# Performance work log

Hardware: AMD Instinct MI355X
Metric: run time of the kernel (lower is better)

The kernel has to match this reference:

```python
import jax, jax.numpy as jnp
import numpy as np

N_ITEMS = 100000
N_INTENTS = 512
H = 128
ALPHA = 0.5
TOPK = 3  # torch code: sim.topk(3, 1)


def _leaky_relu(x):
    return jnp.where(x > 0, x, 0.2 * x)  # nn.LeakyReLU(0.2)


def setup_inputs() -> dict:
    key = jax.random.key(0)
    k0, k1, k2, k3, k4, k5 = jax.random.split(key, 6)
    s = 1.0 / np.sqrt(H)
    return {
        "item_emb": jax.random.normal(k0, (N_ITEMS, H), jnp.float32),
        "intent_emb": jax.random.normal(k1, (N_INTENTS, H), jnp.float32),
        "Wq": (jax.random.normal(k2, (H, H), jnp.float32) * s),  # lq.weight
        "Wk": (jax.random.normal(k3, (H, H), jnp.float32) * s),  # lk.weight
        "wa": (jax.random.normal(k4, (H,), jnp.float32) * s),    # la.weight (1,H)
        "wb": (jax.random.normal(k5, (H,), jnp.float32) * s),    # lb.weight (1,H)
        "n_items": N_ITEMS,
        "n_intents": N_INTENTS,
    }


def reference(item_emb, intent_emb, Wq, Wk, wa, wb, n_items, n_intents):
    h = item_emb.shape[1]
    # dense similarity + row softmax + top-3 sparsification (indices only matter downstream)
    sim = (item_emb @ Wq.T) @ (intent_emb @ Wk.T).T / jnp.sqrt(jnp.float32(h))
    sim = jax.nn.softmax(sim, axis=1)                      # [n_items, n_intents]
    _, topi = jax.lax.top_k(sim, TOPK)                     # [n_items, 3]
    edge_item = jnp.repeat(jnp.arange(n_items), TOPK)      # [E]
    edge_intent = topi.reshape(-1)                         # [E]

    # --- GNNCell ---
    # att1: edges oriented intent<-item, softmax per intent row (segment softmax)
    s1 = _leaky_relu((intent_emb[edge_intent] * item_emb[edge_item]) @ wa)  # [E]
    m1 = jax.ops.segment_max(s1, edge_intent, num_segments=n_intents)
    e1 = jnp.exp(s1 - m1[edge_intent])
    d1 = jax.ops.segment_sum(e1, edge_intent, num_segments=n_intents)
    w1 = e1 / d1[edge_intent]
    intent_new = jax.ops.segment_sum(w1[:, None] * item_emb[edge_item],
                                     edge_intent, num_segments=n_intents)  # [n_intents, H]

    # att2: edges oriented item<-intent; each item has exactly 3 edges -> softmax over axis 1
    s2 = _leaky_relu((item_emb[edge_item] * intent_new[edge_intent]) @ wb)
    w2 = jax.nn.softmax(s2.reshape(n_items, TOPK), axis=1)  # [n_items, 3]
    item_nei = jnp.einsum("nk,nkh->nh", w2, intent_new[topi])

    return ALPHA * item_emb + (1.0 - ALPHA) * item_nei
```

## Files before the change

### kernel.cpp

```cpp
#include <hip/hip_runtime.h>
#include <math.h>

#define N_ITEMS 100000
#define N_INT   512
#define H       128
#define KCH     16
#define NCH     (H/KCH)
#define IPB     16
#define IPW     4
#define TILE    512
#define MAXTILES 2048

typedef unsigned int u32;

__device__ __forceinline__ float wave_sum(float v) {
#pragma unroll
  for (int d = 1; d < 64; d <<= 1) v += __shfl_xor(v, d, 64);
  return v;
}

__global__ void k_projK(const float* __restrict__ intent, const float* __restrict__ Wk,
                        float* __restrict__ K) {
  __shared__ float row[H];
  int j = blockIdx.x, h = threadIdx.x;
  row[h] = intent[j * H + h];
  __syncthreads();
  float acc = 0.f;
#pragma unroll 8
  for (int k = 0; k < H; ++k) acc += row[k] * Wk[h * H + k];
  K[j * H + h] = acc;
}

__global__ void k_projM(const float* __restrict__ Wq, const float* __restrict__ K,
                        float* __restrict__ M) {
  __shared__ float row[H];
  int j = blockIdx.x, k = threadIdx.x;
  row[k] = K[j * H + k];
  __syncthreads();
  float acc = 0.f;
#pragma unroll 8
  for (int a = 0; a < H; ++a) acc += Wq[a * H + k] * row[a];
  M[k * N_INT + j] = acc * 0.08838834764831845f;
}

__global__ __launch_bounds__(256) void k_simtop(
    const float* __restrict__ item, const float* __restrict__ M,
    const float* __restrict__ intent, const float* __restrict__ wa,
    int* __restrict__ topi, float* __restrict__ s1buf, int* __restrict__ counts) {
  __shared__ float sm[KCH * N_INT];
  __shared__ float sit[IPB * KCH];
  const int tid = threadIdx.x;
  const int lane = tid & 63;
  const int wv = __builtin_amdgcn_readfirstlane(tid >> 6);
  const int ibase = blockIdx.x * IPB;
  const int iw = wv * IPW * KCH;

  float acc[IPW][8];
#pragma unroll
  for (int i = 0; i < IPW; ++i)
#pragma unroll
    for (int jj = 0; jj < 8; ++jj) acc[i][jj] = 0.f;

  for (int kc = 0; kc < NCH; ++kc) {
    __syncthreads();
#pragma unroll
    for (int t = 0; t < 8; ++t) {
      int off = wv * 2048 + t * 256;
      __builtin_amdgcn_global_load_lds(
          (const __attribute__((address_space(1))) u32*)(M + kc * (KCH * N_INT) + off + lane * 4),
          (__attribute__((address_space(3))) u32*)(sm + off), 16, 0, 0);
    }
    if (wv == 0) {
      __builtin_amdgcn_global_load_lds(
          (const __attribute__((address_space(1))) u32*)(item + (size_t)(ibase + (lane >> 2)) * H + kc * KCH + (lane & 3) * 4),
          (__attribute__((address_space(3))) u32*)(sit + lane * 4), 16, 0, 0);
    }
    __syncthreads();
#pragma unroll
    for (int q = 0; q < 4; ++q) {
#pragma unroll
      for (int kk = 0; kk < 4; ++kk) {
        const int krow = q * 4 + kk;
        const float* rp = sm + krow * N_INT + lane * 4;
        float4 m0 = *reinterpret_cast<const float4*>(rp);
        float4 m1 = *reinterpret_cast<const float4*>(rp + 256);
#pragma unroll
        for (int i = 0; i < IPW; ++i) {
          float a = sit[iw + i * KCH + krow];
          acc[i][0] += a * m0.x; acc[i][1] += a * m0.y;
          acc[i][2] += a * m0.z; acc[i][3] += a * m0.w;
          acc[i][4] += a * m1.x; acc[i][5] += a * m1.y;
          acc[i][6] += a * m1.z; acc[i][7] += a * m1.w;
        }
      }
    }
  }

  const float wal = wa[lane], wah = wa[64 + lane];
#pragma unroll
  for (int i = 0; i < IPW; ++i) {
    float tv0 = -INFINITY, tv1 = -INFINITY, tv2 = -INFINITY;
    int ti0 = 0x7fffffff, ti1 = 0x7fffffff, ti2 = 0x7fffffff;
    auto push = [&](float v, int j) {
      bool b2 = (v > tv2) || (v == tv2 && j < ti2);
      if (b2) {
        bool b1 = (v > tv1) || (v == tv1 && j < ti1);
        if (b1) {
          bool b0 = (v > tv0) || (v == tv0 && j < ti0);
          if (b0) { tv2 = tv1; ti2 = ti1; tv1 = tv0; ti1 = ti0; tv0 = v; ti0 = j; }
          else    { tv2 = tv1; ti2 = ti1; tv1 = v; ti1 = j; }
        } else    { tv2 = v; ti2 = j; }
      }
    };
#pragma unroll
    for (int jj = 0; jj < 8; ++jj) {
      int j = (jj < 4) ? (4 * lane + jj) : (256 + 4 * lane + (jj - 4));
      push(acc[i][jj], j);
    }
#pragma unroll
    for (int d = 1; d < 64; d <<= 1) {
      float ov0 = __shfl_xor(tv0, d, 64), ov1 = __shfl_xor(tv1, d, 64), ov2 = __shfl_xor(tv2, d, 64);
      int   oi0 = __shfl_xor(ti0, d, 64), oi1 = __shfl_xor(ti1, d, 64), oi2 = __shfl_xor(ti2, d, 64);
      push(ov0, oi0); push(ov1, oi1); push(ov2, oi2);
    }
    const int gi = ibase + wv * IPW + i;
    const float itl = item[(size_t)gi * H + lane], ith = item[(size_t)gi * H + 64 + lane];
    const float pl = itl * wal, ph = ith * wah;
    int jsel[3] = {ti0, ti1, ti2};
#pragma unroll
    for (int e = 0; e < 3; ++e) {
      int j = jsel[e];
      float s = pl * intent[j * H + lane] + ph * intent[j * H + 64 + lane];
      s = wave_sum(s);
      s = (s > 0.f) ? s : 0.2f * s;
      if (lane == 0) {
        topi[gi * 3 + e] = j;
        s1buf[gi * 3 + e] = s;
        atomicAdd(&counts[j], 1);
      }
    }
  }
}

__global__ void k_scan(const int* __restrict__ counts, int* __restrict__ offs,
                       int* __restrict__ cursor, int* __restrict__ descs,
                       int* __restrict__ ntl) {
  __shared__ int s[N_INT];
  __shared__ int base;
  int t = threadIdx.x;
  if (t == 0) base = 0;
  int c = counts[t];
  s[t] = c;
  __syncthreads();
  for (int off = 1; off < N_INT; off <<= 1) {
    int v = (t >= off) ? s[t - off] : 0;
    __syncthreads();
    s[t] += v;
    __syncthreads();
  }
  int excl = s[t] - c;
  offs[t] = excl;
  cursor[t] = excl;
  if (t == N_INT - 1) offs[N_INT] = s[t];
  int nt = (c + TILE - 1) / TILE;
  int my = atomicAdd(&base, nt);
  for (int k = 0; k < nt; ++k) {
    descs[2 * (my + k)] = t;
    descs[2 * (my + k) + 1] = excl + k * TILE;
  }
  __syncthreads();
  if (t == 0) ntl[0] = base;
}

__global__ void k_scatter(const int* __restrict__ topi, const float* __restrict__ s1buf,
                          int* __restrict__ cursor, int* __restrict__ eitem,
                          float* __restrict__ es1) {
  int gi = blockIdx.x * 256 + threadIdx.x;
  if (gi >= N_ITEMS) return;
#pragma unroll
  for (int e = 0; e < 3; ++e) {
    int j = topi[gi * 3 + e];
    int pos = atomicAdd(&cursor[j], 1);
    eitem[pos] = gi;
    es1[pos] = s1buf[gi * 3 + e];
  }
}

__global__ __launch_bounds__(256) void k_agg(
    const float* __restrict__ item, const int* __restrict__ offs,
    const int* __restrict__ descs, const int* __restrict__ ntl,
    const int* __restrict__ eitem, const float* __restrict__ es1,
    float* __restrict__ num, float* __restrict__ denom) {
  int bt = blockIdx.x;
  if (bt >= ntl[0]) return;
  int j = descs[2 * bt];
  int beg = descs[2 * bt + 1];
  int end = min(offs[j + 1], beg + TILE);
  __shared__ float red[256];
  __shared__ float rd[2];
  int t = threadIdx.x;
  int h = t & 127, sub = t >> 7;
  float acc = 0.f, dp = 0.f;
  const float* ip = item + h;
#pragma unroll 4
  for (int e = beg + sub; e < end; e += 2) {
    float e1 = expf(es1[e]);
    acc += e1 * ip[(size_t)eitem[e] * H];
    dp += e1;
  }
  red[t] = acc;
  if (h == 0) rd[sub] = dp;
  __syncthreads();
  if (t < 128) atomicAdd(&num[j * H + t], red[t] + red[t + 128]);
  if (t == 0) atomicAdd(&denom[j], rd[0] + rd[1]);
}

__global__ __launch_bounds__(256) void k_final(
    const float* __restrict__ item, const int* __restrict__ topi,
    const float* __restrict__ num, const float* __restrict__ denom,
    const float* __restrict__ wb, float* __restrict__ out) {
  int tid = threadIdx.x;
  int lane = tid & 63;
  int wv = __builtin_amdgcn_readfirstlane(tid >> 6);
  int gi = blockIdx.x * 4 + wv;
  const float il = item[(size_t)gi * H + lane], ih = item[(size_t)gi * H + 64 + lane];
  const float wbl = wb[lane], wbh = wb[64 + lane];
  int j0 = topi[gi * 3 + 0], j1 = topi[gi * 3 + 1], j2 = topi[gi * 3 + 2];
  float d0 = denom[j0], d1 = denom[j1], d2 = denom[j2];
  float r0 = d0 > 0.f ? 1.f / d0 : 0.f;
  float r1 = d1 > 0.f ? 1.f / d1 : 0.f;
  float r2 = d2 > 0.f ? 1.f / d2 : 0.f;
  float n0l = num[j0 * H + lane] * r0, n0h = num[j0 * H + 64 + lane] * r0;
  float n1l = num[j1 * H + lane] * r1, n1h = num[j1 * H + 64 + lane] * r1;
  float n2l = num[j2 * H + lane] * r2, n2h = num[j2 * H + 64 + lane] * r2;
  float s0 = wave_sum(il * n0l * wbl + ih * n0h * wbh);
  float s1 = wave_sum(il * n1l * wbl + ih * n1h * wbh);
  float s2 = wave_sum(il * n2l * wbl + ih * n2h * wbh);
  s0 = s0 > 0.f ? s0 : 0.2f * s0;
  s1 = s1 > 0.f ? s1 : 0.2f * s1;
  s2 = s2 > 0.f ? s2 : 0.2f * s2;
  float mx = fmaxf(s0, fmaxf(s1, s2));
  float e0 = expf(s0 - mx), e1 = expf(s1 - mx), e2 = expf(s2 - mx);
  float inv = 1.f / (e0 + e1 + e2);
  float w0 = e0 * inv, w1 = e1 * inv, w2 = e2 * inv;
  out[(size_t)gi * H + lane]      = 0.5f * il + 0.5f * (w0 * n0l + w1 * n1l + w2 * n2l);
  out[(size_t)gi * H + 64 + lane] = 0.5f * ih + 0.5f * (w0 * n0h + w1 * n1h + w2 * n2h);
}

extern "C" void kernel_launch(void* const* d_in, const int* in_sizes, int n_in,
                              void* d_out, int out_size, void* d_ws, size_t ws_size,
                              hipStream_t stream) {
  (void)in_sizes; (void)n_in; (void)out_size; (void)ws_size;
  const float* item   = (const float*)d_in[0];
  const float* intent = (const float*)d_in[1];
  const float* Wq     = (const float*)d_in[2];
  const float* Wk     = (const float*)d_in[3];
  const float* wa     = (const float*)d_in[4];
  const float* wb     = (const float*)d_in[5];
  float* out = (float*)d_out;

  char* w = (char*)d_ws;
  auto alloc = [&](size_t bytes) {
    char* p = w;
    w += (bytes + 255) & ~(size_t)255;
    return p;
  };
  float* K      = (float*)alloc(N_INT * H * 4);
  float* M      = (float*)alloc((size_t)H * N_INT * 4);
  int*   topi   = (int*)alloc((size_t)N_ITEMS * 3 * 4);
  float* s1b    = (float*)alloc((size_t)N_ITEMS * 3 * 4);
  int*   offs   = (int*)alloc((N_INT + 1) * 4);
  int*   cursor = (int*)alloc(N_INT * 4);
  int*   eitem  = (int*)alloc((size_t)N_ITEMS * 3 * 4);
  float* es1    = (float*)alloc((size_t)N_ITEMS * 3 * 4);
  int*   descs  = (int*)alloc(MAXTILES * 2 * 4);
  char*  zbase  = w;
  int*   counts = (int*)alloc(N_INT * 4);
  int*   ntl    = (int*)alloc(4);
  float* denom  = (float*)alloc(N_INT * 4);
  float* num    = (float*)alloc(N_INT * H * 4);
  size_t zlen   = (size_t)(w - zbase);

  hipMemsetAsync(zbase, 0, zlen, stream);
  k_projK<<<N_INT, H, 0, stream>>>(intent, Wk, K);
  k_projM<<<N_INT, H, 0, stream>>>(Wq, K, M);
  k_simtop<<<N_ITEMS / IPB, 256, 0, stream>>>(item, M, intent, wa, topi, s1b, counts);
  k_scan<<<1, N_INT, 0, stream>>>(counts, offs, cursor, descs, ntl);
  k_scatter<<<(N_ITEMS + 255) / 256, 256, 0, stream>>>(topi, s1b, cursor, eitem, es1);
  k_agg<<<MAXTILES, 256, 0, stream>>>(item, offs, descs, ntl, eitem, es1, num, denom);
  k_final<<<N_ITEMS / 4, 256, 0, stream>>>(item, topi, num, denom, wb, out);
}
```

Baseline: 982.0 us.

## Drop LDS staging in sim kernel, read M and items directly with more items per wave

The similarity/top-k kernel no longer stages chunks of M and item rows through shared memory with per-chunk barriers. Each wave now loads item float4s and M rows straight from global memory (relying on L1/L2 for the shared M), and handles 8 items per wave instead of 4, which doubles register accumulators and adds an occupancy hint in launch bounds. The three edge-score wave reductions are also interleaved into one shuffle loop. The risk is more global/L2 traffic for M, since each wave reads it independently, and higher register pressure.

```diff
diff --git a/kernel.cpp b/kernel.cpp
--- a/kernel.cpp
+++ b/kernel.cpp
@@ -4,10 +4,8 @@
 #define N_ITEMS 100000
 #define N_INT   512
 #define H       128
-#define KCH     16
-#define NCH     (H/KCH)
-#define IPB     16
-#define IPW     4
+#define IPW     8
+#define IPB     32
 #define TILE    512
 #define MAXTILES 2048
 
@@ -43,17 +41,14 @@
   M[k * N_INT + j] = acc * 0.08838834764831845f;
 }
 
-__global__ __launch_bounds__(256) void k_simtop(
+__global__ __launch_bounds__(256, 3) void k_simtop(
     const float* __restrict__ item, const float* __restrict__ M,
     const float* __restrict__ intent, const float* __restrict__ wa,
     int* __restrict__ topi, float* __restrict__ s1buf, int* __restrict__ counts) {
-  __shared__ float sm[KCH * N_INT];
-  __shared__ float sit[IPB * KCH];
   const int tid = threadIdx.x;
   const int lane = tid & 63;
   const int wv = __builtin_amdgcn_readfirstlane(tid >> 6);
-  const int ibase = blockIdx.x * IPB;
-  const int iw = wv * IPW * KCH;
+  const int ibase = blockIdx.x * IPB + wv * IPW;
 
   float acc[IPW][8];
 #pragma unroll
@@ -61,37 +56,25 @@
 #pragma unroll
     for (int jj = 0; jj < 8; ++jj) acc[i][jj] = 0.f;
 
-  for (int kc = 0; kc < NCH; ++kc) {
-    __syncthreads();
-#pragma unroll
-    for (int t = 0; t < 8; ++t) {
-      int off = wv * 2048 + t * 256;
-      __builtin_amdgcn_global_load_lds(
-          (const __attribute__((address_space(1))) u32*)(M + kc * (KCH * N_INT) + off + lane * 4),
-          (__attribute__((address_space(3))) u32*)(sm + off), 16, 0, 0);
-    }
-    if (wv == 0) {
-      __builtin_amdgcn_global_load_lds(
-          (const __attribute__((address_space(1))) u32*)(item + (size_t)(ibase + (lane >> 2)) * H + kc * KCH + (lane & 3) * 4),
-          (__attribute__((address_space(3))) u32*)(sit + lane * 4), 16, 0, 0);
-    }
-    __syncthreads();
-#pragma unroll
-    for (int q = 0; q < 4; ++q) {
-#pragma unroll
-      for (int kk = 0; kk < 4; ++kk) {
-        const int krow = q * 4 + kk;
-        const float* rp = sm + krow * N_INT + lane * 4;
-        float4 m0 = *reinterpret_cast<const float4*>(rp);
-        float4 m1 = *reinterpret_cast<const float4*>(rp + 256);
-#pragma unroll
-        for (int i = 0; i < IPW; ++i) {
-          float a = sit[iw + i * KCH + krow];
-          acc[i][0] += a * m0.x; acc[i][1] += a * m0.y;
-          acc[i][2] += a * m0.z; acc[i][3] += a * m0.w;
-          acc[i][4] += a * m1.x; acc[i][5] += a * m1.y;
-          acc[i][6] += a * m1.z; acc[i][7] += a * m1.w;
-        }
+  const float* mlane = M + 4 * lane;
+#pragma unroll 2
+  for (int k4 = 0; k4 < H / 4; ++k4) {
+    float4 av[IPW];
+#pragma unroll
+    for (int i = 0; i < IPW; ++i)
+      av[i] = *reinterpret_cast<const float4*>(item + (size_t)(ibase + i) * H + k4 * 4);
+#pragma unroll
+    for (int kk = 0; kk < 4; ++kk) {
+      const float* rp = mlane + (k4 * 4 + kk) * N_INT;
+      float4 m0 = *reinterpret_cast<const float4*>(rp);
+      float4 m1 = *reinterpret_cast<const float4*>(rp + 256);
+#pragma unroll
+      for (int i = 0; i < IPW; ++i) {
+        float a = (kk == 0) ? av[i].x : (kk == 1) ? av[i].y : (kk == 2) ? av[i].z : av[i].w;
+        acc[i][0] += a * m0.x; acc[i][1] += a * m0.y;
+        acc[i][2] += a * m0.z; acc[i][3] += a * m0.w;
+        acc[i][4] += a * m1.x; acc[i][5] += a * m1.y;
+        acc[i][6] += a * m1.z; acc[i][7] += a * m1.w;
       }
     }
   }
@@ -123,21 +106,26 @@
       int   oi0 = __shfl_xor(ti0, d, 64), oi1 = __shfl_xor(ti1, d, 64), oi2 = __shfl_xor(ti2, d, 64);
       push(ov0, oi0); push(ov1, oi1); push(ov2, oi2);
     }
-    const int gi = ibase + wv * IPW + i;
+    const int gi = ibase + i;
     const float itl = item[(size_t)gi * H + lane], ith = item[(size_t)gi * H + 64 + lane];
     const float pl = itl * wal, ph = ith * wah;
-    int jsel[3] = {ti0, ti1, ti2};
-#pragma unroll
-    for (int e = 0; e < 3; ++e) {
-      int j = jsel[e];
-      float s = pl * intent[j * H + lane] + ph * intent[j * H + 64 + lane];
-      s = wave_sum(s);
-      s = (s > 0.f) ? s : 0.2f * s;
-      if (lane == 0) {
-        topi[gi * 3 + e] = j;
-        s1buf[gi * 3 + e] = s;
-        atomicAdd(&counts[j], 1);
-      }
+    float s0 = pl * intent[ti0 * H + lane] + ph * intent[ti0 * H + 64 + lane];
+    float s1 = pl * intent[ti1 * H + lane] + ph * intent[ti1 * H + 64 + lane];
+    float s2 = pl * intent[ti2 * H + lane] + ph * intent[ti2 * H + 64 + lane];
+#pragma unroll
+    for (int d = 1; d < 64; d <<= 1) {
+      float t0 = __shfl_xor(s0, d, 64);
+      float t1 = __shfl_xor(s1, d, 64);
+      float t2 = __shfl_xor(s2, d, 64);
+      s0 += t0; s1 += t1; s2 += t2;
+    }
+    s0 = (s0 > 0.f) ? s0 : 0.2f * s0;
+    s1 = (s1 > 0.f) ? s1 : 0.2f * s1;
+    s2 = (s2 > 0.f) ? s2 : 0.2f * s2;
+    if (lane == 0) {
+      topi[gi * 3 + 0] = ti0; s1buf[gi * 3 + 0] = s0; atomicAdd(&counts[ti0], 1);
+      topi[gi * 3 + 1] = ti1; s1buf[gi * 3 + 1] = s1; atomicAdd(&counts[ti1], 1);
+      topi[gi * 3 + 2] = ti2; s1buf[gi * 3 + 2] = s2; atomicAdd(&counts[ti2], 1);
     }
   }
 }
```

New measurement: 818.6 us. 16.6% less time.
